# Kernel tuning notes

Hardware: AMD Instinct MI355X
Metric: run time of the kernel (lower is better)

The kernel has to match this reference:

```python
import jax, jax.numpy as jnp
import numpy as np

GROUP_SIZE = 128


def dequantize_int4(packed, scales, group_size=GROUP_SIZE, dtype=jnp.float16):
    # packed: [O, I//2] bytes; low nibble -> even cols, high nibble -> odd cols
    O = packed.shape[0]
    I = packed.shape[1] * 2
    low = (packed & 15).astype(jnp.int8) - 8
    high = ((packed >> 4) & 15).astype(jnp.int8) - 8
    unpacked = jnp.stack([low, high], axis=-1).reshape(O, I)  # interleave low/high
    G = I // group_size
    grouped = unpacked.reshape(O, G, group_size).astype(jnp.float32)
    deq = grouped * scales.astype(jnp.float32)[:, :, None]  # per-group scale
    return deq.reshape(O, I).astype(dtype)


def setup_inputs() -> dict:
    key = jax.random.key(0)
    k1, k2, k3 = jax.random.split(key, 3)
    B, S, IN, OUT = 4, 2048, 4096, 11008
    G = IN // GROUP_SIZE
    x = jax.random.normal(k1, (B, S, IN), dtype=jnp.float16)
    packed = jax.random.randint(k2, (OUT, IN // 2), 0, 256, dtype=jnp.int32)
    scales = (jax.random.uniform(k3, (OUT, G), dtype=jnp.float32) * 0.05 + 0.001).astype(jnp.float16)
    return {"x": x, "packed": packed, "scales": scales}


def reference(x, packed, scales):
    x = x.astype(jnp.float16)
    W = dequantize_int4(packed, scales)  # [OUT, IN] fp16
    # nn.functional.linear: x @ W^T
    return jnp.einsum('bsi,oi->bso', x, W)
```

## Files before the change

### kernel.cpp

```cpp
#include <hip/hip_runtime.h>

#define M_DIM 8192
#define N_DIM 11008
#define K_DIM 4096
#define GROUPS 32
#define WQROW 512
#define LDSK 72

typedef short s16x8 __attribute__((ext_vector_type(8)));
typedef _Float16 f16x8 __attribute__((ext_vector_type(8)));
typedef _Float16 h2 __attribute__((ext_vector_type(2)));
typedef float f32x4 __attribute__((ext_vector_type(4)));
typedef unsigned short u16;
typedef unsigned int u32;

union f32u { float f; unsigned u; };
union h16u { u16 u; _Float16 h; };

__device__ __forceinline__ u16 f2bf(float f) {
  f32u v; v.f = f;
  unsigned r = v.u + 0x7FFFu + ((v.u >> 16) & 1u);
  return (u16)(r >> 16);
}
__device__ __forceinline__ float bf2f(u16 b) {
  f32u v; v.u = ((unsigned)b) << 16; return v.f;
}
__device__ __forceinline__ float h2f(u16 b) {
  h16u v; v.u = b; return (float)v.h;
}

__global__ void probe_mode_kernel(const void* __restrict__ scales,
                                  int* __restrict__ mode_out) {
  __shared__ int cnt[3];
  int t = threadIdx.x;
  if (t < 3) cnt[t] = 0;
  __syncthreads();
  float f0 = ((const float*)scales)[t];
  u16  hu  = ((const u16*)scales)[t];
  float f1 = h2f(hu);
  float f2 = bf2f(hu);
  if (f0 > 0.0004f && f0 < 0.065f) atomicAdd(&cnt[0], 1);
  if (f1 > 0.0004f && f1 < 0.065f) atomicAdd(&cnt[1], 1);
  if (f2 > 0.0004f && f2 < 0.065f) atomicAdd(&cnt[2], 1);
  __syncthreads();
  if (t == 0) {
    int m;
    if      (cnt[1] >= 240) m = 1;
    else if (cnt[2] >= 240) m = 2;
    else                    m = 0;
    mode_out[0] = m;
  }
}

__global__ __launch_bounds__(256) void convert_x_nat_kernel(
    const float* __restrict__ xf, u16* __restrict__ xh,
    const int* __restrict__ modep) {
  if (modep && modep[0] != 0) return;
  const int total8 = M_DIM * (K_DIM / 8);
  int idx = blockIdx.x * 256 + threadIdx.x;
  const int stride = gridDim.x * 256;
  for (; idx < total8; idx += stride) {
    const float4* p = (const float4*)(xf + (size_t)idx * 8);
    float4 a = p[0], b = p[1];
    union { _Float16 h[8]; s16x8 v; } r;
    r.h[0] = (_Float16)a.x; r.h[1] = (_Float16)a.y;
    r.h[2] = (_Float16)a.z; r.h[3] = (_Float16)a.w;
    r.h[4] = (_Float16)b.x; r.h[5] = (_Float16)b.y;
    r.h[6] = (_Float16)b.z; r.h[7] = (_Float16)b.w;
    *(s16x8*)(xh + (size_t)idx * 8) = r.v;
  }
}

__global__ __launch_bounds__(256) void dequant_w_kernel(
    const int* __restrict__ packed, const float* __restrict__ scf,
    u16* __restrict__ wf, const int* __restrict__ modep) {
  if (modep && modep[0] != 0) return;
  const int total = N_DIM * (K_DIM / 8);
  int idx = blockIdx.x * 256 + threadIdx.x;
  const int stride = gridDim.x * 256;
  for (; idx < total; idx += stride) {
    const int col = idx >> 9;
    const int d   = idx & 511;
    const float s = scf[col * GROUPS + (d >> 4)];
    const int4 p  = ((const int4*)packed)[idx];
    const int vals[4] = {p.x, p.y, p.z, p.w};
    union { _Float16 h[8]; s16x8 v; } r;
    #pragma unroll
    for (int e = 0; e < 4; ++e) {
      int b = vals[e] & 255;
      r.h[2 * e]     = (_Float16)((float)((b & 15) - 8) * s);
      r.h[2 * e + 1] = (_Float16)((float)(((b >> 4) & 15) - 8) * s);
    }
    *(s16x8*)(wf + (size_t)idx * 8) = r.v;
  }
}

__global__ __launch_bounds__(512, 2) void q4gemm_big_kernel(
    const u16* __restrict__ xh,
    const u16* __restrict__ wf,
    float* __restrict__ out,
    const int* __restrict__ modep)
{
  if (modep && modep[0] != 0) return;

  __shared__ _Float16 AsA[2][256 * 64];
  __shared__ _Float16 AsB[2][256 * 64];

  const int tid  = threadIdx.x;
  const int lane = tid & 63;
  const int wv   = tid >> 6;
  const int wm   = (wv >> 2) * 128;
  const int wn   = (wv & 3) * 64;
  const int ln15 = lane & 15;
  const int lk   = lane >> 4;

  int bid = blockIdx.x;
  int f   = (bid & 7) * 172 + (bid >> 3);
  int bn  = f / 32;
  int bm  = f - bn * 32;
  const int m0 = bm * 256;
  const int n0 = bn * 256;

  const int srow  = lane >> 3;
  const int sperm = (lane & 7) ^ srow;
  const u16* abase[4];
  const u16* bbase[4];
  #pragma unroll
  for (int q = 0; q < 4; ++q) {
    int row = q * 64 + wv * 8 + srow;
    abase[q] = xh + (size_t)(m0 + row) * K_DIM + sperm * 8;
    bbase[q] = wf + (size_t)(n0 + row) * K_DIM + sperm * 8;
  }

#define STAGE_ALL(PB, T) do { \
    _Float16* da = &AsA[(PB)][0]; \
    _Float16* db = &AsB[(PB)][0]; \
    _Pragma("unroll") \
    for (int q = 0; q < 4; ++q) \
      __builtin_amdgcn_global_load_lds( \
          (const __attribute__((address_space(1))) void*)(abase[q] + (T) * 64), \
          (__attribute__((address_space(3))) void*)(da + q * 4096 + wv * 512), \
          16, 0, 0); \
    _Pragma("unroll") \
    for (int q = 0; q < 4; ++q) \
      __builtin_amdgcn_global_load_lds( \
          (const __attribute__((address_space(1))) void*)(bbase[q] + (T) * 64), \
          (__attribute__((address_space(3))) void*)(db + q * 4096 + wv * 512), \
          16, 0, 0); \
  } while (0)

  f32x4 acc[8][4];
  #pragma unroll
  for (int i = 0; i < 8; ++i)
    #pragma unroll
    for (int j = 0; j < 4; ++j)
      acc[i][j] = f32x4{0.f, 0.f, 0.f, 0.f};

  STAGE_ALL(0, 0);

  #pragma unroll 1
  for (int t = 0; t < 64; ++t) {
    const int cur = t & 1;

    asm volatile("s_waitcnt vmcnt(0)" ::: "memory");
    __builtin_amdgcn_s_barrier();

    if (t < 63) STAGE_ALL(cur ^ 1, t + 1);

    const _Float16* Ab = &AsA[cur][0];
    const _Float16* Bb = &AsB[cur][0];
    const int slotx = ln15 & 7;

    #pragma unroll
    for (int kkc = 0; kkc < 2; ++kkc) {
      const int slot = (kkc * 4 + lk) ^ slotx;
      f16x8 bf[4];
      #pragma unroll
      for (int j = 0; j < 4; ++j) {
        int r = wn + j * 16 + ln15;
        bf[j] = *(const f16x8*)&Bb[r * 64 + slot * 8];
      }
      #pragma unroll
      for (int ih = 0; ih < 2; ++ih) {
        f16x8 af[4];
        #pragma unroll
        for (int ii = 0; ii < 4; ++ii) {
          int r = wm + (ih * 4 + ii) * 16 + ln15;
          af[ii] = *(const f16x8*)&Ab[r * 64 + slot * 8];
        }
        __builtin_amdgcn_s_barrier();
        asm volatile("s_waitcnt lgkmcnt(0)" ::: "memory");
        __builtin_amdgcn_sched_barrier(0);
        __builtin_amdgcn_s_setprio(1);
        #pragma unroll
        for (int ii = 0; ii < 4; ++ii) {
          acc[ih * 4 + ii][0] = __builtin_amdgcn_mfma_f32_16x16x32_f16(af[ii], bf[0], acc[ih * 4 + ii][0], 0, 0, 0);
          acc[ih * 4 + ii][1] = __builtin_amdgcn_mfma_f32_16x16x32_f16(af[ii], bf[1], acc[ih * 4 + ii][1], 0, 0, 0);
          acc[ih * 4 + ii][2] = __builtin_amdgcn_mfma_f32_16x16x32_f16(af[ii], bf[2], acc[ih * 4 + ii][2], 0, 0, 0);
          acc[ih * 4 + ii][3] = __builtin_amdgcn_mfma_f32_16x16x32_f16(af[ii], bf[3], acc[ih * 4 + ii][3], 0, 0, 0);
        }
        __builtin_amdgcn_s_setprio(0);
        __builtin_amdgcn_s_barrier();
      }
    }
  }

  #pragma unroll
  for (int i = 0; i < 8; ++i) {
    int r0 = m0 + wm + i * 16 + (lane >> 4) * 4;
    #pragma unroll
    for (int j = 0; j < 4; ++j) {
      int cc = n0 + wn + j * 16 + ln15;
      #pragma unroll
      for (int r = 0; r < 4; ++r)
        __builtin_nontemporal_store(acc[i][j][r], &out[(size_t)(r0 + r) * N_DIM + cc]);
    }
  }
#undef STAGE_ALL
}

__global__ __launch_bounds__(256) void convert_x_perm_kernel(
    const float* __restrict__ xf, u16* __restrict__ xh,
    const int* __restrict__ modep) {
  if (modep && modep[0] != 0) return;
  const int total8 = M_DIM * (K_DIM / 8);
  int idx = blockIdx.x * 256 + threadIdx.x;
  const int stride = gridDim.x * 256;
  for (; idx < total8; idx += stride) {
    const float4* p = (const float4*)(xf + (size_t)idx * 8);
    float4 a = p[0], b = p[1];
    union { _Float16 h[8]; s16x8 v; } r;
    r.h[0] = (_Float16)a.x; r.h[1] = (_Float16)b.x;
    r.h[2] = (_Float16)a.y; r.h[3] = (_Float16)b.y;
    r.h[4] = (_Float16)a.z; r.h[5] = (_Float16)b.z;
    r.h[6] = (_Float16)a.w; r.h[7] = (_Float16)b.w;
    *(s16x8*)(xh + (size_t)idx * 8) = r.v;
  }
}

__global__ __launch_bounds__(256) void repack_w_kernel(
    const int* __restrict__ packed, u32* __restrict__ wq) {
  const int total = N_DIM * WQROW;
  int idx = blockIdx.x * 256 + threadIdx.x;
  const int stride = gridDim.x * 256;
  for (; idx < total; idx += stride) {
    const int4 p = ((const int4*)packed)[idx];
    wq[idx] = (u32)(p.x & 255) | ((u32)(p.y & 255) << 8) |
              ((u32)(p.z & 255) << 16) | ((u32)p.w << 24);
  }
}

__device__ __forceinline__ f16x8 dq8(u32 q, h2 s2) {
  const u32 M = 0x000F000Fu, G = 0x64006400u;
  const h2 bias = {(_Float16)(-1032.0f), (_Float16)(-1032.0f)};
  union { u32 u; h2 h; } a0, a1, a2, a3;
  a0.u = (q & M) | G;
  a1.u = ((q >> 4) & M) | G;
  a2.u = ((q >> 8) & M) | G;
  a3.u = ((q >> 12) & M) | G;
  a0.h = (a0.h + bias) * s2;
  a1.h = (a1.h + bias) * s2;
  a2.h = (a2.h + bias) * s2;
  a3.h = (a3.h + bias) * s2;
  union { u32 u[4]; f16x8 f; } r;
  r.u[0] = a0.u; r.u[1] = a1.u; r.u[2] = a2.u; r.u[3] = a3.u;
  return r.f;
}

__global__ __launch_bounds__(256, 2) void q4gemm_mid_kernel(
    const u16* __restrict__ xh, const u32* __restrict__ wq,
    const float* __restrict__ scf, float* __restrict__ out,
    const int* __restrict__ modep)
{
  if (modep && modep[0] != 0) return;

  __shared__ _Float16 As[3][128 * 64];

  const int tid  = threadIdx.x;
  const int lane = tid & 63;
  const int wv   = tid >> 6;
  const int wn   = wv * 64;
  const int ln15 = lane & 15;
  const int lk   = lane >> 4;

  int bid = blockIdx.x;
  int f   = (bid & 7) * 344 + (bid >> 3);
  int bn  = f / 64;
  int bm  = f - bn * 64;
  const int m0 = bm * 128;
  const int n0 = bn * 256;

  const u16* abase[4];
  #pragma unroll
  for (int q = 0; q < 4; ++q) {
    int row = q * 32 + wv * 8 + (lane >> 3);
    abase[q] = xh + (size_t)(m0 + row) * K_DIM + (((lane & 7) ^ (lane >> 3)) * 8);
  }

#define STAGE(PB, T) do { \
    _Float16* dst = &As[(PB)][0]; \
    _Pragma("unroll") \
    for (int q = 0; q < 4; ++q) \
      __builtin_amdgcn_global_load_lds( \
          (const __attribute__((address_space(1))) void*)(abase[q] + (T) * 64), \
          (__attribute__((address_space(3))) void*)(dst + q * 2048 + wv * 512), \
          16, 0, 0); \
  } while (0)

#define LOADB(RB, T) do { \
    _Pragma("unroll") \
    for (int j = 0; j < 4; ++j) { \
      RB[j]     = wq[pcol[j] + (T) * 8]; \
      RB[j + 4] = wq[pcol[j] + (T) * 8 + 4]; \
    } \
  } while (0)

#define COMPUTE(RB, PB) do { \
    const _Float16* asb = &As[(PB)][0]; \
    _Pragma("unroll") \
    for (int kkc = 0; kkc < 2; ++kkc) { \
      f16x8 bfr0 = dq8(RB[kkc * 4 + 0], s2[0]); \
      f16x8 bfr1 = dq8(RB[kkc * 4 + 1], s2[1]); \
      f16x8 bfr2 = dq8(RB[kkc * 4 + 2], s2[2]); \
      f16x8 bfr3 = dq8(RB[kkc * 4 + 3], s2[3]); \
      _Pragma("unroll") \
      for (int i = 0; i < 8; ++i) { \
        const int row  = i * 16 + ln15; \
        const int slot = (kkc * 4 + lk) ^ (ln15 & 7); \
        f16x8 af = *(const f16x8*)&asb[row * 64 + slot * 8]; \
        acc[i][0] = __builtin_amdgcn_mfma_f32_16x16x32_f16(af, bfr0, acc[i][0], 0, 0, 0); \
        acc[i][1] = __builtin_amdgcn_mfma_f32_16x16x32_f16(af, bfr1, acc[i][1], 0, 0, 0); \
        acc[i][2] = __builtin_amdgcn_mfma_f32_16x16x32_f16(af, bfr2, acc[i][2], 0, 0, 0); \
        acc[i][3] = __builtin_amdgcn_mfma_f32_16x16x32_f16(af, bfr3, acc[i][3], 0, 0, 0); \
      } \
    } \
  } while (0)

  int pcol[4], scol[4];
  #pragma unroll
  for (int j = 0; j < 4; ++j) {
    int col = n0 + wn + j * 16 + ln15;
    pcol[j] = col * WQROW + lk;
    scol[j] = col * GROUPS;
  }

  f32x4 acc[8][4];
  #pragma unroll
  for (int i = 0; i < 8; ++i)
    #pragma unroll
    for (int j = 0; j < 4; ++j)
      acc[i][j] = f32x4{0.f, 0.f, 0.f, 0.f};

  u32 rbE[8], rbO[8];
  float snextf[4];
  h2 s2[4];

  STAGE(0, 0);
  STAGE(1, 1);
  LOADB(rbE, 0);
  LOADB(rbO, 1);
  #pragma unroll
  for (int j = 0; j < 4; ++j) snextf[j] = scf[scol[j]];
  asm volatile("s_waitcnt vmcnt(0)" ::: "memory");

  int p0 = 0, p1 = 1, p2 = 2;

  for (int tp = 0; tp < 32; ++tp) {
    const int t0 = 2 * tp;
    const int t1 = t0 + 1;

    asm volatile("s_waitcnt vmcnt(12)" ::: "memory");
    __builtin_amdgcn_s_barrier();
    __builtin_amdgcn_sched_barrier(0);

    #pragma unroll
    for (int j = 0; j < 4; ++j) {
      _Float16 sh = (_Float16)snextf[j];
      s2[j] = h2{sh, sh};
    }
    if (t0 + 2 < 64) STAGE(p2, t0 + 2);

    __builtin_amdgcn_s_setprio(1);
    COMPUTE(rbE, p0);
    __builtin_amdgcn_s_setprio(0);

    if (t0 + 2 < 64) LOADB(rbE, t0 + 2);
    {
      const int gn = (tp + 1 > 31) ? 31 : (tp + 1);
      #pragma unroll
      for (int j = 0; j < 4; ++j) snextf[j] = scf[scol[j] + gn];
    }

    if (tp == 31) {
      asm volatile("s_waitcnt vmcnt(0)" ::: "memory");
    } else {
      asm volatile("s_waitcnt vmcnt(12)" ::: "memory");
    }
    __builtin_amdgcn_s_barrier();
    __builtin_amdgcn_sched_barrier(0);

    if (t1 + 2 < 64) STAGE(p0, t1 + 2);

    __builtin_amdgcn_s_setprio(1);
    COMPUTE(rbO, p1);
    __builtin_amdgcn_s_setprio(0);

    if (t1 + 2 < 64) LOADB(rbO, t1 + 2);

    int tmp = p2; p2 = p1; p1 = p0; p0 = tmp;
  }

  #pragma unroll
  for (int i = 0; i < 8; ++i) {
    int r0 = m0 + i * 16 + (lane >> 4) * 4;
    #pragma unroll
    for (int j = 0; j < 4; ++j) {
      int cc = n0 + wn + j * 16 + ln15;
      #pragma unroll
      for (int r = 0; r < 4; ++r)
        out[(size_t)(r0 + r) * N_DIM + cc] = acc[i][j][r];
    }
  }
#undef STAGE
#undef LOADB
#undef COMPUTE
}

__global__ __launch_bounds__(256) void q4gemm_slow_kernel(
    const void* __restrict__ xraw,
    const int*  __restrict__ packed,
    const void* __restrict__ scraw,
    float* __restrict__ out,
    const int* __restrict__ modep,
    int skip0)
{
  const int mode = modep ? modep[0] : 0;
  if (skip0 && mode == 0) return;

  __shared__ u16 Asl[128 * LDSK];
  __shared__ u16 Bsl[128 * LDSK];

  const int tid  = threadIdx.x;
  const int lane = tid & 63;
  const int wv   = tid >> 6;
  const int wm   = (wv >> 1) * 64;
  const int wn   = (wv & 1) * 64;
  const int n0   = blockIdx.x * 128;
  const int m0   = blockIdx.y * 128;

  f32x4 acc[4][4];
  #pragma unroll
  for (int i = 0; i < 4; ++i)
    #pragma unroll
    for (int j = 0; j < 4; ++j)
      acc[i][j] = f32x4{0.f, 0.f, 0.f, 0.f};

  const int lrow16 = lane & 15;
  const int lk8    = (lane >> 4) * 8;

  for (int k0 = 0; k0 < K_DIM; k0 += 64) {
    if (mode == 0) {
      const float* xf = (const float*)xraw;
      #pragma unroll
      for (int it = 0; it < 4; ++it) {
        int s = tid + it * 256;
        int row = s >> 3, c8 = (s & 7) * 8;
        const float4* p = (const float4*)(xf + (size_t)(m0 + row) * K_DIM + k0 + c8);
        float4 v0 = p[0], v1 = p[1];
        u16 tmp[8] = { f2bf(v0.x), f2bf(v0.y), f2bf(v0.z), f2bf(v0.w),
                       f2bf(v1.x), f2bf(v1.y), f2bf(v1.z), f2bf(v1.w) };
        *(s16x8*)&Asl[row * LDSK + c8] = *(const s16x8*)tmp;
      }
    } else if (mode == 1) {
      const u16* xhh = (const u16*)xraw;
      #pragma unroll
      for (int it = 0; it < 4; ++it) {
        int s = tid + it * 256;
        int row = s >> 3, c8 = (s & 7) * 8;
        s16x8 v = *(const s16x8*)(xhh + (size_t)(m0 + row) * K_DIM + k0 + c8);
        u16 tmp[8];
        #pragma unroll
        for (int j = 0; j < 8; ++j) tmp[j] = f2bf(h2f((u16)v[j]));
        *(s16x8*)&Asl[row * LDSK + c8] = *(const s16x8*)tmp;
      }
    } else {
      const u16* xhh = (const u16*)xraw;
      #pragma unroll
      for (int it = 0; it < 4; ++it) {
        int s = tid + it * 256;
        int row = s >> 3, c8 = (s & 7) * 8;
        s16x8 v = *(const s16x8*)(xhh + (size_t)(m0 + row) * K_DIM + k0 + c8);
        *(s16x8*)&Asl[row * LDSK + c8] = v;
      }
    }

    {
      int row  = tid >> 1;
      int half = tid & 1;
      int srw  = n0 + row;
      int g    = k0 >> 7;
      float scale;
      if      (mode == 0) scale = ((const float*)scraw)[(size_t)srw * GROUPS + g];
      else if (mode == 1) scale = h2f(((const u16*)scraw)[(size_t)srw * GROUPS + g]);
      else                scale = bf2f(((const u16*)scraw)[(size_t)srw * GROUPS + g]);

      const int4* pp = (const int4*)(packed + (size_t)srw * (K_DIM / 2) + (k0 >> 1) + half * 16);
      #pragma unroll
      for (int j = 0; j < 4; ++j) {
        int4 pv = pp[j];
        int vals[4] = {pv.x, pv.y, pv.z, pv.w};
        u16 w[8];
        #pragma unroll
        for (int e = 0; e < 4; ++e) {
          int b = vals[e] & 255;
          w[e * 2]     = f2bf(scale * (float)((b & 15) - 8));
          w[e * 2 + 1] = f2bf(scale * (float)(((b >> 4) & 15) - 8));
        }
        int i0 = half * 16 + j * 4;
        *(s16x8*)&Bsl[row * LDSK + i0 * 2] = *(const s16x8*)w;
      }
    }
    __syncthreads();

    #pragma unroll
    for (int kk = 0; kk < 64; kk += 32) {
      s16x8 af[4], bfr[4];
      int klane = kk + lk8;
      #pragma unroll
      for (int i = 0; i < 4; ++i)
        af[i] = *(const s16x8*)&Asl[(wm + i * 16 + lrow16) * LDSK + klane];
      #pragma unroll
      for (int i = 0; i < 4; ++i)
        bfr[i] = *(const s16x8*)&Bsl[(wn + i * 16 + lrow16) * LDSK + klane];
      #pragma unroll
      for (int i = 0; i < 4; ++i)
        #pragma unroll
        for (int j = 0; j < 4; ++j)
          acc[i][j] = __builtin_amdgcn_mfma_f32_16x16x32_bf16(af[i], bfr[j], acc[i][j], 0, 0, 0);
    }
    __syncthreads();
  }

  #pragma unroll
  for (int i = 0; i < 4; ++i) {
    int rbase = m0 + wm + i * 16 + ((lane >> 4) * 4);
    #pragma unroll
    for (int j = 0; j < 4; ++j) {
      int c = n0 + wn + j * 16 + (lane & 15);
      #pragma unroll
      for (int r = 0; r < 4; ++r)
        out[(size_t)(rbase + r) * N_DIM + c] = acc[i][j][r];
    }
  }
}

extern "C" void kernel_launch(void* const* d_in, const int* in_sizes, int n_in,
                              void* d_out, int out_size, void* d_ws, size_t ws_size,
                              hipStream_t stream) {
  const void* x      = d_in[0];
  const int*  packed = (const int*)d_in[1];
  const void* scales = d_in[2];
  float* out = (float*)d_out;

  const size_t XB = (size_t)M_DIM * K_DIM * 2;
  const size_t WF = (size_t)N_DIM * K_DIM * 2;
  const size_t WQ = (size_t)N_DIM * WQROW * 4;
  const size_t NEED_BIG = 256 + XB + WF;
  const size_t NEED_MID = 256 + XB + WQ;

  int* mode_flag = nullptr;
  if (ws_size >= 4) {
    mode_flag = (int*)d_ws;
    probe_mode_kernel<<<dim3(1), dim3(256), 0, stream>>>(scales, mode_flag);
  }

  int fast = 0;
  if (mode_flag && ws_size >= NEED_BIG) fast = 2;
  else if (mode_flag && ws_size >= NEED_MID) fast = 1;

  if (fast == 2) {
    u16* xh = (u16*)((char*)d_ws + 256);
    u16* wf = (u16*)((char*)d_ws + 256 + XB);
    convert_x_nat_kernel<<<dim3(2048), dim3(256), 0, stream>>>(
        (const float*)x, xh, mode_flag);
    dequant_w_kernel<<<dim3(2048), dim3(256), 0, stream>>>(
        packed, (const float*)scales, wf, mode_flag);
    q4gemm_big_kernel<<<dim3(1376), dim3(512), 0, stream>>>(
        xh, wf, out, mode_flag);
  } else if (fast == 1) {
    u16* xh = (u16*)((char*)d_ws + 256);
    u32* wq = (u32*)((char*)d_ws + 256 + XB);
    convert_x_perm_kernel<<<dim3(2048), dim3(256), 0, stream>>>(
        (const float*)x, xh, mode_flag);
    repack_w_kernel<<<dim3(2048), dim3(256), 0, stream>>>(packed, wq);
    q4gemm_mid_kernel<<<dim3(2752), dim3(256), 0, stream>>>(
        xh, wq, (const float*)scales, out, mode_flag);
  }

  q4gemm_slow_kernel<<<dim3(N_DIM / 128, M_DIM / 128), dim3(256), 0, stream>>>(
      x, packed, scales, out, mode_flag, fast);
}
```

Measured before the change: 967.3 us.

## Software-pipeline LDS fragment loads with MFMA and drop intra-tile barriers

Restructures the inner K-tile loop so LDS reads for the next fragment batch are issued while the current MFMA batch runs, using double register fragments (bf0/bf1, afA/afB) and sched_barriers to fix ordering. It removes the per-subtile s_barrier pairs and explicit lgkmcnt(0) waits, which serialized waves and stalled MFMA issue. In exchange it raises VGPR pressure for the extra fragments, and it relies on compiler-inserted waitcnts for correctness.

```diff
diff --git a/kernel.cpp b/kernel.cpp
--- a/kernel.cpp
+++ b/kernel.cpp
@@ -149,6 +149,34 @@
           16, 0, 0); \
   } while (0)
 
+#define LOAD_AF(DST, IH, SLOT) do { \
+    _Pragma("unroll") \
+    for (int ii = 0; ii < 4; ++ii) { \
+      int r = wm + ((IH) * 4 + ii) * 16 + ln15; \
+      DST[ii] = *(const f16x8*)&Ab[r * 64 + (SLOT) * 8]; \
+    } \
+  } while (0)
+
+#define LOAD_BF(DST, SLOT) do { \
+    _Pragma("unroll") \
+    for (int j = 0; j < 4; ++j) { \
+      int r = wn + j * 16 + ln15; \
+      DST[j] = *(const f16x8*)&Bb[r * 64 + (SLOT) * 8]; \
+    } \
+  } while (0)
+
+#define MFMA16(AF, BF, IH) do { \
+    __builtin_amdgcn_s_setprio(1); \
+    _Pragma("unroll") \
+    for (int ii = 0; ii < 4; ++ii) { \
+      acc[(IH) * 4 + ii][0] = __builtin_amdgcn_mfma_f32_16x16x32_f16(AF[ii], BF[0], acc[(IH) * 4 + ii][0], 0, 0, 0); \
+      acc[(IH) * 4 + ii][1] = __builtin_amdgcn_mfma_f32_16x16x32_f16(AF[ii], BF[1], acc[(IH) * 4 + ii][1], 0, 0, 0); \
+      acc[(IH) * 4 + ii][2] = __builtin_amdgcn_mfma_f32_16x16x32_f16(AF[ii], BF[2], acc[(IH) * 4 + ii][2], 0, 0, 0); \
+      acc[(IH) * 4 + ii][3] = __builtin_amdgcn_mfma_f32_16x16x32_f16(AF[ii], BF[3], acc[(IH) * 4 + ii][3], 0, 0, 0); \
+    } \
+    __builtin_amdgcn_s_setprio(0); \
+  } while (0)
+
   f32x4 acc[8][4];
   #pragma unroll
   for (int i = 0; i < 8; ++i)
@@ -170,39 +198,25 @@
     const _Float16* Ab = &AsA[cur][0];
     const _Float16* Bb = &AsB[cur][0];
     const int slotx = ln15 & 7;
-
-    #pragma unroll
-    for (int kkc = 0; kkc < 2; ++kkc) {
-      const int slot = (kkc * 4 + lk) ^ slotx;
-      f16x8 bf[4];
-      #pragma unroll
-      for (int j = 0; j < 4; ++j) {
-        int r = wn + j * 16 + ln15;
-        bf[j] = *(const f16x8*)&Bb[r * 64 + slot * 8];
-      }
-      #pragma unroll
-      for (int ih = 0; ih < 2; ++ih) {
-        f16x8 af[4];
-        #pragma unroll
-        for (int ii = 0; ii < 4; ++ii) {
-          int r = wm + (ih * 4 + ii) * 16 + ln15;
-          af[ii] = *(const f16x8*)&Ab[r * 64 + slot * 8];
-        }
-        __builtin_amdgcn_s_barrier();
-        asm volatile("s_waitcnt lgkmcnt(0)" ::: "memory");
-        __builtin_amdgcn_sched_barrier(0);
-        __builtin_amdgcn_s_setprio(1);
-        #pragma unroll
-        for (int ii = 0; ii < 4; ++ii) {
-          acc[ih * 4 + ii][0] = __builtin_amdgcn_mfma_f32_16x16x32_f16(af[ii], bf[0], acc[ih * 4 + ii][0], 0, 0, 0);
-          acc[ih * 4 + ii][1] = __builtin_amdgcn_mfma_f32_16x16x32_f16(af[ii], bf[1], acc[ih * 4 + ii][1], 0, 0, 0);
-          acc[ih * 4 + ii][2] = __builtin_amdgcn_mfma_f32_16x16x32_f16(af[ii], bf[2], acc[ih * 4 + ii][2], 0, 0, 0);
-          acc[ih * 4 + ii][3] = __builtin_amdgcn_mfma_f32_16x16x32_f16(af[ii], bf[3], acc[ih * 4 + ii][3], 0, 0, 0);
-        }
-        __builtin_amdgcn_s_setprio(0);
-        __builtin_amdgcn_s_barrier();
-      }
-    }
+    const int slot0 = lk ^ slotx;
+    const int slot1 = (4 + lk) ^ slotx;
+
+    f16x8 bf0[4], bf1[4], afA[4], afB[4];
+
+    LOAD_BF(bf0, slot0);
+    LOAD_AF(afA, 0, slot0);
+    LOAD_AF(afB, 1, slot0);
+    __builtin_amdgcn_sched_barrier(0);
+    MFMA16(afA, bf0, 0);
+    LOAD_BF(bf1, slot1);
+    LOAD_AF(afA, 0, slot1);
+    __builtin_amdgcn_sched_barrier(0);
+    MFMA16(afB, bf0, 1);
+    LOAD_AF(afB, 1, slot1);
+    __builtin_amdgcn_sched_barrier(0);
+    MFMA16(afA, bf1, 0);
+    __builtin_amdgcn_sched_barrier(0);
+    MFMA16(afB, bf1, 1);
   }
 
   #pragma unroll
@@ -217,6 +231,9 @@
     }
   }
 #undef STAGE_ALL
+#undef LOAD_AF
+#undef LOAD_BF
+#undef MFMA16
 }
 
 __global__ __launch_bounds__(256) void convert_x_perm_kernel(
```

Measured after the change: 839.3 us. 1.15x faster.
